# Kernel tuning notes

Hardware: AMD Instinct MI355X
Metric: run time of the kernel (lower is better)

The kernel has to match this reference:

```python
import jax, jax.numpy as jnp
import numpy as np

B, N, CIN, COUT, P = 16, 10000, 8, 32, 8
E = 160000
TRAIN_OR_PREDICT = 1


def setup_inputs() -> dict:
    key = jax.random.key(0)
    ks = jax.random.split(key, 12)
    inp = {}
    inp["X"] = jax.random.normal(ks[0], (B, N, CIN, 2 * P), dtype=jnp.float32)
    inp["edge_index"] = jax.random.randint(ks[1], (2, E), 0, N, dtype=jnp.int64)
    inp["edge_weight"] = jax.random.uniform(ks[2], (E,), dtype=jnp.float32)
    inp["attention"] = jax.random.uniform(ks[3], (2 * P,), dtype=jnp.float32)
    sc = 1.0 / np.sqrt(CIN)
    sl = 1.0 / np.sqrt(2 * COUT)
    names = ["z", "r", "h"]
    for i, g in enumerate(names):
        inp["Wc" + g] = jax.random.normal(ks[4 + i], (CIN, COUT), dtype=jnp.float32) * sc
        inp["bc" + g] = jnp.zeros((COUT,), dtype=jnp.float32)
        inp["Wl" + g] = jax.random.normal(ks[7 + i], (2 * COUT, COUT), dtype=jnp.float32) * sl
        inp["bl" + g] = jnp.zeros((COUT,), dtype=jnp.float32)
    return inp


def _gcn_norm(edge_index, edge_weight, n):
    # PyG gcn_norm: add self-loops (weight 1.0), symmetric D^-1/2 (A+I) D^-1/2
    src, dst = edge_index[0], edge_index[1]
    loop = jnp.arange(n)
    src = jnp.concatenate([src, loop])
    dst = jnp.concatenate([dst, loop])
    w = jnp.concatenate([edge_weight, jnp.ones((n,), edge_weight.dtype)])
    deg = jax.ops.segment_sum(w, dst, num_segments=n)
    dinv = jnp.where(deg > 0, deg ** -0.5, 0.0)
    return src, dst, dinv[src] * w * dinv[dst]


def _gcn(X, W, b, src, dst, norm, n):
    # propagate-then-transform: (A_hat X) W + b  (linear, identical to X W then A_hat)
    msg = X[:, src, :] * norm[None, :, None]                     # (B, E', Cin)
    agg = jax.ops.segment_sum(jnp.swapaxes(msg, 0, 1), dst, num_segments=n)  # (N, B, Cin)
    return jnp.einsum('bni,io->bno', jnp.swapaxes(agg, 0, 1), W) + b


def reference(X, edge_index, edge_weight, attention,
              Wcz, bcz, Wlz, blz, Wcr, bcr, Wlr, blr, Wch, bch, Wlh, blh):
    b_, n, _, t2 = X.shape
    p = t2 // 2
    src, dst, norm = _gcn_norm(edge_index, edge_weight, n)
    probs = jax.nn.softmax(attention)
    # backward half of the sum is scaled by TrainorPredict (linearity of the weighted sum)
    ws = jnp.concatenate([probs[:p], probs[p:] * TRAIN_OR_PREDICT])
    H0 = jnp.zeros((b_, n, Wlz.shape[1]), X.dtype)
    Xs = jnp.moveaxis(X, 3, 0)  # (2P, B, N, Cin); H is never chained in the original loop

    def cell(x):
        Z = jax.nn.sigmoid(jnp.concatenate([_gcn(x, Wcz, bcz, src, dst, norm, n), H0], -1) @ Wlz + blz)
        R = jax.nn.sigmoid(jnp.concatenate([_gcn(x, Wcr, bcr, src, dst, norm, n), H0], -1) @ Wlr + blr)
        Ht = jnp.tanh(jnp.concatenate([_gcn(x, Wch, bch, src, dst, norm, n), H0 * R], -1) @ Wlh + blh)
        return Z * H0 + (1.0 - Z) * Ht

    def step(acc, pw):
        x, w = pw
        return acc + w * cell(x), None

    out, _ = jax.lax.scan(step, H0, (Xs, ws))
    return out
```

## Files before the change

### kernel.cpp

```cpp
#include <hip/hip_runtime.h>
#include <stdint.h>

#define NN 10000
#define NE 160000
#define NB 16
#define NT 4

typedef __attribute__((ext_vector_type(8))) float f32x8;
typedef __attribute__((ext_vector_type(4))) float f32x4;
typedef __attribute__((ext_vector_type(2))) float f32x2;
typedef __attribute__((ext_vector_type(8))) _Float16 h16x8;

#define AGG_LD 136

__device__ __forceinline__ int ei_stride(const int* __restrict__ ei) {
    int z = ei[1] | ei[3] | ei[5] | ei[7] | ei[9] | ei[11] | ei[13] | ei[15];
    return (z == 0) ? 2 : 1;
}

__global__ __launch_bounds__(256)
void k_prep(const float* __restrict__ X, h16x8* __restrict__ X2, int do_repack,
            const int* __restrict__ ei, const float* __restrict__ ew,
            float* deg, int* count,
            const float* __restrict__ attn,
            const float* __restrict__ Wcz, const float* __restrict__ bcz,
            const float* __restrict__ Wlz, const float* __restrict__ blz,
            const float* __restrict__ Wch, const float* __restrict__ bch,
            const float* __restrict__ Wlh, const float* __restrict__ blh,
            float* consts) {
    int gid = blockIdx.x * blockDim.x + threadIdx.x;
    int gsz = gridDim.x * blockDim.x;
    int stride = ei_stride(ei);
    for (int e = gid; e < NE; e += gsz) {
        int d = ei[(size_t)(NE + e) * stride];
        atomicAdd(&deg[d], ew[e]);
        atomicAdd(&count[d], 1);
    }
    if (do_repack) {
        const int total = NN * 256;
        for (int i = gid; i < total; i += gsz) {
            int n = i >> 8, t = i & 255;
            int b = t >> 4, chunk = t & 15;
            f32x8 w = ((const f32x8*)X)[((size_t)b * NN + n) * 16 + chunk];
            h16x8 h;
            #pragma unroll
            for (int j = 0; j < 8; ++j) h[j] = (_Float16)w[j];
            X2[((size_t)(b >> 1) * NN + n) * 32 + (b & 1) * 16 + chunk] = h;
        }
    }
    if (blockIdx.x == 0) {
        int tid = threadIdx.x;
        {
            int c = tid >> 5, o = tid & 31;
            float mz = 0.f, mh = 0.f;
            for (int k = 0; k < 32; ++k) {
                mz += Wcz[c * 32 + k] * Wlz[k * 32 + o];
                mh += Wch[c * 32 + k] * Wlh[k * 32 + o];
            }
            consts[tid] = mz;
            consts[256 + tid] = mh;
        }
        if (tid < 32) {
            float cz = blz[tid], ch = blh[tid];
            for (int k = 0; k < 32; ++k) {
                cz += bcz[k] * Wlz[k * 32 + tid];
                ch += bch[k] * Wlh[k * 32 + tid];
            }
            consts[512 + tid] = cz;
            consts[544 + tid] = ch;
        }
        if (tid == 0) {
            float a[16], m = -1e30f, s = 0.f;
            for (int t = 0; t < 16; ++t) { a[t] = attn[t]; m = fmaxf(m, a[t]); }
            for (int t = 0; t < 16; ++t) { a[t] = __expf(a[t] - m); s += a[t]; }
            for (int t = 0; t < 16; ++t) consts[576 + t] = a[t] / s;
        }
    }
}

__global__ void k_scan(const float* __restrict__ deg, const int* __restrict__ count,
                       float* dinv, int* offsets, int* fillptr) {
    int tid = threadIdx.x;
    int lane = tid & 63, wv = tid >> 6;
    __shared__ int wsum[16];
    __shared__ int carry;
    if (tid == 0) carry = 0;
    __syncthreads();
    for (int base = 0; base < NN; base += 1024) {
        int i = base + tid;
        int v = (i < NN) ? count[i] : 0;
        int x = v;
        #pragma unroll
        for (int s = 1; s < 64; s <<= 1) {
            int y = __shfl_up(x, s, 64);
            if (lane >= s) x += y;
        }
        if (lane == 63) wsum[wv] = x;
        __syncthreads();
        if (wv == 0 && lane < 16) {
            int y = wsum[lane];
            #pragma unroll
            for (int s = 1; s < 16; s <<= 1) {
                int z = __shfl_up(y, s, 64);
                if (lane >= s) y += z;
            }
            wsum[lane] = y;
        }
        __syncthreads();
        int wbase = (wv == 0) ? 0 : wsum[wv - 1];
        int incl = carry + wbase + x;
        int excl = incl - v;
        if (i < NN) { offsets[i] = excl; fillptr[i] = excl; }
        __syncthreads();
        if (tid == 1023) carry = incl;
        __syncthreads();
    }
    for (int i = tid; i < NN; i += 1024) dinv[i] = rsqrtf(deg[i] + 1.0f);
}

__global__ void k_fill(const int* __restrict__ ei, const float* __restrict__ ew,
                       const float* __restrict__ dinv,
                       int* fillptr, int* csr_src, float* csr_norm) {
    int e = blockIdx.x * blockDim.x + threadIdx.x;
    if (e >= NE) return;
    int stride = ei_stride(ei);
    int s = ei[(size_t)e * stride];
    int d = ei[(size_t)(NE + e) * stride];
    int pos = atomicAdd(&fillptr[d], 1);
    csr_src[pos] = s;
    csr_norm[pos] = dinv[s] * ew[e] * dinv[d];
}

__device__ __forceinline__ float gatefn(float uz, float uh) {
    float ez = __expf(uz);
    float eh = __expf(2.f * uh);
    return (eh - 1.f) * __builtin_amdgcn_rcpf((1.f + ez) * (eh + 1.f));
}

__global__ __launch_bounds__(256)
void k_main_h(const h16x8* __restrict__ X2,
              const int* __restrict__ offsets, const int* __restrict__ count,
              const float* __restrict__ dinv,
              const int* __restrict__ csr_src, const float* __restrict__ csr_norm,
              const float* __restrict__ consts,
              float* __restrict__ out) {
    __shared__ float sAgg[2 * NT * AGG_LD];
    __shared__ float sMz[256], sMh[256], sCz[32], sCh[32], sWs[16];
    int tid = threadIdx.x;
    int bp   = blockIdx.x & 7;
    int tile = blockIdx.x >> 3;

    sMz[tid] = consts[tid];
    sMh[tid] = consts[256 + tid];
    if (tid < 32) { sCz[tid] = consts[512 + tid]; sCh[tid] = consts[544 + tid]; }
    if (tid < 16) sWs[tid] = consts[576 + tid];

    int lane = tid & 63;
    int wv = __builtin_amdgcn_readfirstlane(tid >> 6);
    int half = lane >> 5;
    int chunk = lane & 31;
    int n = tile * NT + wv;
    const h16x8* xb = X2 + ((size_t)bp * NN) * 32;
    float dn = dinv[n];
    float selfn = (half == 0) ? dn * dn : 0.f;
    float acc[8];
    {
        h16x8 w = xb[(size_t)n * 32 + chunk];
        #pragma unroll
        for (int j = 0; j < 8; ++j) acc[j] = selfn * (float)w[j];
    }
    int off = offsets[n], cnt = count[n];
    const int*   sp  = csr_src + off;
    const float* npv = csr_norm + off;
    int e = 0;
    if (cnt >= 8) {
        int s0 = sp[0], s1 = sp[1], s2 = sp[2], s3 = sp[3];
        int sa = half ? s1 : s0, sb = half ? s3 : s2;
        h16x8 a0 = xb[(size_t)sa * 32 + chunk];
        h16x8 a1 = xb[(size_t)sb * 32 + chunk];
        for (e = 4; e + 4 <= cnt; e += 4) {
            int t0 = sp[e], t1 = sp[e + 1], t2 = sp[e + 2], t3 = sp[e + 3];
            int ta = half ? t1 : t0, tb = half ? t3 : t2;
            h16x8 b0 = xb[(size_t)ta * 32 + chunk];
            h16x8 b1 = xb[(size_t)tb * 32 + chunk];
            __builtin_amdgcn_sched_barrier(0);
            float n0 = npv[e - 4], n1 = npv[e - 3], n2 = npv[e - 2], n3 = npv[e - 1];
            float na = half ? n1 : n0, nb = half ? n3 : n2;
            #pragma unroll
            for (int j = 0; j < 8; ++j) acc[j] += na * (float)a0[j];
            #pragma unroll
            for (int j = 0; j < 8; ++j) acc[j] += nb * (float)a1[j];
            a0 = b0; a1 = b1;
        }
        float n0 = npv[e - 4], n1 = npv[e - 3], n2 = npv[e - 2], n3 = npv[e - 1];
        float na = half ? n1 : n0, nb = half ? n3 : n2;
        #pragma unroll
        for (int j = 0; j < 8; ++j) acc[j] += na * (float)a0[j];
        #pragma unroll
        for (int j = 0; j < 8; ++j) acc[j] += nb * (float)a1[j];
    }
    for (; e + 2 <= cnt; e += 2) {
        int s0 = sp[e], s1 = sp[e + 1];
        int sa = half ? s1 : s0;
        float n0 = npv[e], n1 = npv[e + 1];
        float na = half ? n1 : n0;
        h16x8 w = xb[(size_t)sa * 32 + chunk];
        #pragma unroll
        for (int j = 0; j < 8; ++j) acc[j] += na * (float)w[j];
    }
    if (e < cnt) {
        int s = sp[e];
        float nrm = half ? 0.f : npv[e];
        h16x8 w = xb[(size_t)s * 32 + chunk];
        #pragma unroll
        for (int j = 0; j < 8; ++j) acc[j] += nrm * (float)w[j];
    }
    #pragma unroll
    for (int j = 0; j < 8; ++j) acc[j] += __shfl_xor(acc[j], 32);
    if (lane < 32) {
        int bl = chunk >> 4;
        int sub = chunk & 15;
        int r = wv * 2 + bl;
        int c = sub >> 1;
        int tpb = (sub & 1) * 4;
        float* rowp = &sAgg[r * AGG_LD + c * 2];
        #pragma unroll
        for (int k = 0; k < 4; ++k) {
            f32x2 v = {acc[2 * k], acc[2 * k + 1]};
            *(f32x2*)&rowp[(tpb + k) * 16] = v;
        }
    }
    __syncthreads();

    int o = tid & 31, rr = tid >> 5;
    float mz[8], mh[8];
    #pragma unroll
    for (int c = 0; c < 8; ++c) { mz[c] = sMz[c * 32 + o]; mh[c] = sMh[c * 32 + o]; }
    float czo = sCz[o], cho = sCh[o];
    const f32x4* r0 = (const f32x4*)&sAgg[rr * AGG_LD];
    f32x2 o0 = {0.f, 0.f};
    #pragma unroll
    for (int tp = 0; tp < 8; ++tp) {
        f32x4 A0[4];
        #pragma unroll
        for (int k = 0; k < 4; ++k) A0[k] = r0[tp * 4 + k];
        f32x2 uz = {czo, czo}, uh = {cho, cho};
        #pragma unroll
        for (int k = 0; k < 4; ++k) {
            f32x2 p = A0[k].xy, q = A0[k].zw;
            uz += p * mz[2 * k]; uz += q * mz[2 * k + 1];
            uh += p * mh[2 * k]; uh += q * mh[2 * k + 1];
        }
        f32x2 wsp = {sWs[2 * tp], sWs[2 * tp + 1]};
        f32x2 g;
        g.x = gatefn(uz.x, uh.x);
        g.y = gatefn(uz.y, uh.y);
        o0 += wsp * g;
    }
    int b  = bp * 2 + (rr & 1);
    int n2 = tile * NT + (rr >> 1);
    out[((size_t)b * NN + n2) * 32 + o] = o0.x + o0.y;
}

__global__ __launch_bounds__(256)
void k_main_f32(const float* __restrict__ X,
                const int* __restrict__ offsets, const int* __restrict__ count,
                const float* __restrict__ dinv,
                const int* __restrict__ csr_src, const float* __restrict__ csr_norm,
                const float* __restrict__ consts,
                float* __restrict__ out) {
    __shared__ float sAgg[NB * 128];
    __shared__ float sMz[256], sMh[256], sCz[32], sCh[32], sWs[16];
    int tid = threadIdx.x;
    int n = blockIdx.x;

    sMz[tid] = consts[tid];
    sMh[tid] = consts[256 + tid];
    if (tid < 32) { sCz[tid] = consts[512 + tid]; sCh[tid] = consts[544 + tid]; }
    if (tid < 16) sWs[tid] = consts[576 + tid];

    int b = tid >> 4, chunk = tid & 15;
    const f32x8* xv = (const f32x8*)X;
    float dn = dinv[n];
    float selfn = dn * dn;
    float acc[8];
    {
        f32x8 w = xv[((size_t)b * NN + n) * 16 + chunk];
        #pragma unroll
        for (int j = 0; j < 8; ++j) acc[j] = selfn * w[j];
    }
    int off = offsets[n], cnt = count[n];
    for (int e = off; e < off + cnt; ++e) {
        int s = csr_src[e];
        float nrm = csr_norm[e];
        f32x8 w = xv[((size_t)b * NN + s) * 16 + chunk];
        #pragma unroll
        for (int j = 0; j < 8; ++j) acc[j] += nrm * w[j];
    }
    #pragma unroll
    for (int j = 0; j < 8; ++j) sAgg[tid * 8 + j] = acc[j];
    __syncthreads();

    int o = tid & 31, b0 = tid >> 5;
    float mz[8], mh[8];
    #pragma unroll
    for (int c = 0; c < 8; ++c) { mz[c] = sMz[c * 32 + o]; mh[c] = sMh[c * 32 + o]; }
    float czo = sCz[o], cho = sCh[o];
    float acc0 = 0.f, acc1 = 0.f;
    #pragma unroll
    for (int t = 0; t < 16; ++t) {
        float uz0 = czo, uh0 = cho, uz1 = czo, uh1 = cho;
        #pragma unroll
        for (int c = 0; c < 8; ++c) {
            float a0 = sAgg[b0 * 128 + c * 16 + t];
            float a1 = sAgg[(b0 + 8) * 128 + c * 16 + t];
            uz0 += a0 * mz[c]; uh0 += a0 * mh[c];
            uz1 += a1 * mz[c]; uh1 += a1 * mh[c];
        }
        float w = sWs[t];
        acc0 += w * gatefn(uz0, uh0);
        acc1 += w * gatefn(uz1, uh1);
    }
    out[((size_t)b0 * NN + n) * 32 + o]       = acc0;
    out[((size_t)(b0 + 8) * NN + n) * 32 + o] = acc1;
}

extern "C" void kernel_launch(void* const* d_in, const int* in_sizes, int n_in,
                              void* d_out, int out_size, void* d_ws, size_t ws_size,
                              hipStream_t stream) {
    const float* X    = (const float*)d_in[0];
    const int*   ei   = (const int*)d_in[1];
    const float* ew   = (const float*)d_in[2];
    const float* attn = (const float*)d_in[3];
    const float* Wcz  = (const float*)d_in[4];
    const float* bcz  = (const float*)d_in[5];
    const float* Wlz  = (const float*)d_in[6];
    const float* blz  = (const float*)d_in[7];
    const float* Wch  = (const float*)d_in[12];
    const float* bch  = (const float*)d_in[13];
    const float* Wlh  = (const float*)d_in[14];
    const float* blh  = (const float*)d_in[15];
    float* out = (float*)d_out;

    const size_t x2_bytes = (size_t)NN * 256 * 16;
    const size_t small_bytes = (size_t)NN * 4 * 5 + (size_t)NE * 4 * 2 + 592 * 4;
    bool use_h = (ws_size >= x2_bytes + small_bytes);

    char* p = (char*)d_ws;
    h16x8* X2 = nullptr;
    if (use_h) { X2 = (h16x8*)p; p += x2_bytes; }
    float* deg      = (float*)p; p += NN * 4;
    int*   count    = (int*)p;   p += NN * 4;
    float* dinv     = (float*)p; p += NN * 4;
    int*   offsets  = (int*)p;   p += NN * 4;
    int*   fillptr  = (int*)p;   p += NN * 4;
    int*   csr_src  = (int*)p;   p += NE * 4;
    float* csr_norm = (float*)p; p += NE * 4;
    float* consts   = (float*)p; p += 592 * 4;

    hipMemsetAsync(deg, 0, (size_t)NN * 8, stream);
    hipLaunchKernelGGL(k_prep, dim3(1280), dim3(256), 0, stream,
                       X, X2, use_h ? 1 : 0, ei, ew, deg, count,
                       attn, Wcz, bcz, Wlz, blz, Wch, bch, Wlh, blh, consts);
    hipLaunchKernelGGL(k_scan, dim3(1), dim3(1024), 0, stream,
                       deg, count, dinv, offsets, fillptr);
    hipLaunchKernelGGL(k_fill, dim3((NE + 255) / 256), dim3(256), 0, stream,
                       ei, ew, dinv, fillptr, csr_src, csr_norm);
    if (use_h) {
        hipLaunchKernelGGL(k_main_h, dim3((NN / NT) * 8), dim3(256), 0, stream,
                           X2, offsets, count, dinv, csr_src, csr_norm, consts, out);
    } else {
        hipLaunchKernelGGL(k_main_f32, dim3(NN), dim3(256), 0, stream,
                           X, offsets, count, dinv, csr_src, csr_norm, consts, out);
    }
}
```

Baseline: 154.0 us.

## Interleave CSR src/norm and deepen gather pipeline to eight edges per step

Stores each CSR edge as an interleaved (pre-scaled source offset, norm) pair, so one array stream serves both values and the multiply by 32 is done once at fill time. The half-precision main kernel now processes eight edges per iteration with four outstanding gathers. It prefetches the next two groups of edge records into registers, and the edge offset and count are made wave-uniform with readfirstlane. The aim is to hide gather latency and cut index-load instructions, at the cost of higher register pressure that could lower occupancy.

```diff
diff --git a/kernel.cpp b/kernel.cpp
--- a/kernel.cpp
+++ b/kernel.cpp
@@ -120,15 +120,15 @@
 
 __global__ void k_fill(const int* __restrict__ ei, const float* __restrict__ ew,
                        const float* __restrict__ dinv,
-                       int* fillptr, int* csr_src, float* csr_norm) {
+                       int* fillptr, int* csr_sn) {
     int e = blockIdx.x * blockDim.x + threadIdx.x;
     if (e >= NE) return;
     int stride = ei_stride(ei);
     int s = ei[(size_t)e * stride];
     int d = ei[(size_t)(NE + e) * stride];
     int pos = atomicAdd(&fillptr[d], 1);
-    csr_src[pos] = s;
-    csr_norm[pos] = dinv[s] * ew[e] * dinv[d];
+    csr_sn[2 * pos]     = s * 32;
+    csr_sn[2 * pos + 1] = __float_as_int(dinv[s] * ew[e] * dinv[d]);
 }
 
 __device__ __forceinline__ float gatefn(float uz, float uh) {
@@ -141,7 +141,7 @@
 void k_main_h(const h16x8* __restrict__ X2,
               const int* __restrict__ offsets, const int* __restrict__ count,
               const float* __restrict__ dinv,
-              const int* __restrict__ csr_src, const float* __restrict__ csr_norm,
+              const int* __restrict__ csr_sn,
               const float* __restrict__ consts,
               float* __restrict__ out) {
     __shared__ float sAgg[2 * NT * AGG_LD];
@@ -169,61 +169,82 @@
         #pragma unroll
         for (int j = 0; j < 8; ++j) acc[j] = selfn * (float)w[j];
     }
-    int off = offsets[n], cnt = count[n];
-    const int*   sp  = csr_src + off;
-    const float* npv = csr_norm + off;
+    int off = __builtin_amdgcn_readfirstlane(offsets[n]);
+    int cnt = __builtin_amdgcn_readfirstlane(count[n]);
+    const int* snp = csr_sn + 2 * off;
     int e = 0;
     if (cnt >= 8) {
-        int s0 = sp[0], s1 = sp[1], s2 = sp[2], s3 = sp[3];
-        int sa = half ? s1 : s0, sb = half ? s3 : s2;
-        h16x8 a0 = xb[(size_t)sa * 32 + chunk];
-        h16x8 a1 = xb[(size_t)sb * 32 + chunk];
-        for (e = 4; e + 4 <= cnt; e += 4) {
-            int t0 = sp[e], t1 = sp[e + 1], t2 = sp[e + 2], t3 = sp[e + 3];
-            int ta = half ? t1 : t0, tb = half ? t3 : t2;
-            h16x8 b0 = xb[(size_t)ta * 32 + chunk];
-            h16x8 b1 = xb[(size_t)tb * 32 + chunk];
+        int p[16], q[16], r[16];
+        #pragma unroll
+        for (int k = 0; k < 16; ++k) p[k] = snp[k];
+        h16x8 A0 = xb[(size_t)(half ? p[2]  : p[0])  + chunk];
+        h16x8 A1 = xb[(size_t)(half ? p[6]  : p[4])  + chunk];
+        h16x8 A2 = xb[(size_t)(half ? p[10] : p[8])  + chunk];
+        h16x8 A3 = xb[(size_t)(half ? p[14] : p[12]) + chunk];
+        #pragma unroll
+        for (int k = 0; k < 16; ++k) q[k] = snp[16 + k];
+        for (e = 8; e + 8 <= cnt; e += 8) {
+            h16x8 B0 = xb[(size_t)(half ? q[2]  : q[0])  + chunk];
+            h16x8 B1 = xb[(size_t)(half ? q[6]  : q[4])  + chunk];
+            h16x8 B2 = xb[(size_t)(half ? q[10] : q[8])  + chunk];
+            h16x8 B3 = xb[(size_t)(half ? q[14] : q[12]) + chunk];
+            #pragma unroll
+            for (int k = 0; k < 16; ++k) r[k] = snp[2 * e + 16 + k];
+            float na0 = __int_as_float(half ? p[3]  : p[1]);
+            float na1 = __int_as_float(half ? p[7]  : p[5]);
+            float na2 = __int_as_float(half ? p[11] : p[9]);
+            float na3 = __int_as_float(half ? p[15] : p[13]);
             __builtin_amdgcn_sched_barrier(0);
-            float n0 = npv[e - 4], n1 = npv[e - 3], n2 = npv[e - 2], n3 = npv[e - 1];
-            float na = half ? n1 : n0, nb = half ? n3 : n2;
-            #pragma unroll
-            for (int j = 0; j < 8; ++j) acc[j] += na * (float)a0[j];
-            #pragma unroll
-            for (int j = 0; j < 8; ++j) acc[j] += nb * (float)a1[j];
-            a0 = b0; a1 = b1;
-        }
-        float n0 = npv[e - 4], n1 = npv[e - 3], n2 = npv[e - 2], n3 = npv[e - 1];
-        float na = half ? n1 : n0, nb = half ? n3 : n2;
-        #pragma unroll
-        for (int j = 0; j < 8; ++j) acc[j] += na * (float)a0[j];
-        #pragma unroll
-        for (int j = 0; j < 8; ++j) acc[j] += nb * (float)a1[j];
+            #pragma unroll
+            for (int j = 0; j < 8; ++j) acc[j] += na0 * (float)A0[j];
+            #pragma unroll
+            for (int j = 0; j < 8; ++j) acc[j] += na1 * (float)A1[j];
+            #pragma unroll
+            for (int j = 0; j < 8; ++j) acc[j] += na2 * (float)A2[j];
+            #pragma unroll
+            for (int j = 0; j < 8; ++j) acc[j] += na3 * (float)A3[j];
+            A0 = B0; A1 = B1; A2 = B2; A3 = B3;
+            #pragma unroll
+            for (int k = 0; k < 16; ++k) { p[k] = q[k]; q[k] = r[k]; }
+        }
+        {
+            float na0 = __int_as_float(half ? p[3]  : p[1]);
+            float na1 = __int_as_float(half ? p[7]  : p[5]);
+            float na2 = __int_as_float(half ? p[11] : p[9]);
+            float na3 = __int_as_float(half ? p[15] : p[13]);
+            #pragma unroll
+            for (int j = 0; j < 8; ++j) acc[j] += na0 * (float)A0[j];
+            #pragma unroll
+            for (int j = 0; j < 8; ++j) acc[j] += na1 * (float)A1[j];
+            #pragma unroll
+            for (int j = 0; j < 8; ++j) acc[j] += na2 * (float)A2[j];
+            #pragma unroll
+            for (int j = 0; j < 8; ++j) acc[j] += na3 * (float)A3[j];
+        }
     }
     for (; e + 2 <= cnt; e += 2) {
-        int s0 = sp[e], s1 = sp[e + 1];
-        int sa = half ? s1 : s0;
-        float n0 = npv[e], n1 = npv[e + 1];
-        float na = half ? n1 : n0;
-        h16x8 w = xb[(size_t)sa * 32 + chunk];
+        int sa   = half ? snp[2 * e + 2] : snp[2 * e];
+        float na = __int_as_float(half ? snp[2 * e + 3] : snp[2 * e + 1]);
+        h16x8 w = xb[(size_t)sa + chunk];
         #pragma unroll
         for (int j = 0; j < 8; ++j) acc[j] += na * (float)w[j];
     }
     if (e < cnt) {
-        int s = sp[e];
-        float nrm = half ? 0.f : npv[e];
-        h16x8 w = xb[(size_t)s * 32 + chunk];
-        #pragma unroll
-        for (int j = 0; j < 8; ++j) acc[j] += nrm * (float)w[j];
+        int sa = snp[2 * e];
+        float na = half ? 0.f : __int_as_float(snp[2 * e + 1]);
+        h16x8 w = xb[(size_t)sa + chunk];
+        #pragma unroll
+        for (int j = 0; j < 8; ++j) acc[j] += na * (float)w[j];
     }
     #pragma unroll
     for (int j = 0; j < 8; ++j) acc[j] += __shfl_xor(acc[j], 32);
     if (lane < 32) {
         int bl = chunk >> 4;
         int sub = chunk & 15;
-        int r = wv * 2 + bl;
+        int rr = wv * 2 + bl;
         int c = sub >> 1;
         int tpb = (sub & 1) * 4;
-        float* rowp = &sAgg[r * AGG_LD + c * 2];
+        float* rowp = &sAgg[rr * AGG_LD + c * 2];
         #pragma unroll
         for (int k = 0; k < 4; ++k) {
             f32x2 v = {acc[2 * k], acc[2 * k + 1]};
@@ -247,9 +268,9 @@
         f32x2 uz = {czo, czo}, uh = {cho, cho};
         #pragma unroll
         for (int k = 0; k < 4; ++k) {
-            f32x2 p = A0[k].xy, q = A0[k].zw;
-            uz += p * mz[2 * k]; uz += q * mz[2 * k + 1];
-            uh += p * mh[2 * k]; uh += q * mh[2 * k + 1];
+            f32x2 pv = A0[k].xy, qv = A0[k].zw;
+            uz += pv * mz[2 * k]; uz += qv * mz[2 * k + 1];
+            uh += pv * mh[2 * k]; uh += qv * mh[2 * k + 1];
         }
         f32x2 wsp = {sWs[2 * tp], sWs[2 * tp + 1]};
         f32x2 g;
@@ -266,7 +287,7 @@
 void k_main_f32(const float* __restrict__ X,
                 const int* __restrict__ offsets, const int* __restrict__ count,
                 const float* __restrict__ dinv,
-                const int* __restrict__ csr_src, const float* __restrict__ csr_norm,
+                const int* __restrict__ csr_sn,
                 const float* __restrict__ consts,
                 float* __restrict__ out) {
     __shared__ float sAgg[NB * 128];
@@ -291,9 +312,9 @@
     }
     int off = offsets[n], cnt = count[n];
     for (int e = off; e < off + cnt; ++e) {
-        int s = csr_src[e];
-        float nrm = csr_norm[e];
-        f32x8 w = xv[((size_t)b * NN + s) * 16 + chunk];
+        int s32 = csr_sn[2 * e];
+        float nrm = __int_as_float(csr_sn[2 * e + 1]);
+        f32x8 w = xv[(size_t)b * NN * 16 + (size_t)(s32 >> 1) + chunk];
         #pragma unroll
         for (int j = 0; j < 8; ++j) acc[j] += nrm * w[j];
     }
@@ -343,7 +364,7 @@
     float* out = (float*)d_out;
 
     const size_t x2_bytes = (size_t)NN * 256 * 16;
-    const size_t small_bytes = (size_t)NN * 4 * 5 + (size_t)NE * 4 * 2 + 592 * 4;
+    const size_t small_bytes = (size_t)NN * 4 * 5 + (size_t)NE * 8 + 592 * 4;
     bool use_h = (ws_size >= x2_bytes + small_bytes);
 
     char* p = (char*)d_ws;
@@ -354,8 +375,7 @@
     float* dinv     = (float*)p; p += NN * 4;
     int*   offsets  = (int*)p;   p += NN * 4;
     int*   fillptr  = (int*)p;   p += NN * 4;
-    int*   csr_src  = (int*)p;   p += NE * 4;
-    float* csr_norm = (float*)p; p += NE * 4;
+    int*   csr_sn   = (int*)p;   p += (size_t)NE * 8;
     float* consts   = (float*)p; p += 592 * 4;
 
     hipMemsetAsync(deg, 0, (size_t)NN * 8, stream);
@@ -365,12 +385,12 @@
     hipLaunchKernelGGL(k_scan, dim3(1), dim3(1024), 0, stream,
                        deg, count, dinv, offsets, fillptr);
     hipLaunchKernelGGL(k_fill, dim3((NE + 255) / 256), dim3(256), 0, stream,
-                       ei, ew, dinv, fillptr, csr_src, csr_norm);
+                       ei, ew, dinv, fillptr, csr_sn);
     if (use_h) {
         hipLaunchKernelGGL(k_main_h, dim3((NN / NT) * 8), dim3(256), 0, stream,
-                           X2, offsets, count, dinv, csr_src, csr_norm, consts, out);
+                           X2, offsets, count, dinv, csr_sn, consts, out);
     } else {
         hipLaunchKernelGGL(k_main_f32, dim3(NN), dim3(256), 0, stream,
-                           X, offsets, count, dinv, csr_src, csr_norm, consts, out);
-    }
-}
+                           X, offsets, count, dinv, csr_sn, consts, out);
+    }
+}
```

Measured after the change: 155.1 us. No clear change (+0.7%).
